# Kernel tuning notes

Measured on AMD Instinct MI355X. Metric: run time of the kernel, lower is better.

Reference implementation:

```python
import jax, jax.numpy as jnp
import numpy as np

STATIC_TH = 0.05
TRIM_RATIO = 0.2
EPS = 1e-6


def setup_inputs() -> dict:
    key = jax.random.key(0)
    k1, k2, k3 = jax.random.split(key, 3)
    B, T, H, W = 2, 32, 518, 518
    pred_disp = jax.random.uniform(k1, (B, T, H, W), jnp.float32, 0.01, 10.0)
    gt_depth = jax.random.uniform(k2, (B, T, H, W), jnp.float32, 0.1, 80.0)
    mask = jax.random.uniform(k3, (B, T, H, W)) > 0.2
    return {"pred_disp": pred_disp, "gt_depth": gt_depth, "mask": mask}


def _nanquantile_rows(vals, valid, q):
    """torch.nanquantile(dim=1, interpolation='linear') where invalid entries are NaN.
    vals: [N,Q] float, valid: [N,Q] bool. Returns [N] threshold (NaN if row empty)."""
    big = jnp.where(valid, vals, jnp.inf)          # invalid -> +inf, sorts to the end
    srt = jnp.sort(big, axis=1)                    # [N,Q]
    nv = valid.sum(axis=1)                         # valid count per row
    pos = q * jnp.maximum(nv - 1, 0).astype(vals.dtype)
    lo = jnp.floor(pos).astype(jnp.int32)
    hi = jnp.ceil(pos).astype(jnp.int32)
    frac = pos - lo.astype(vals.dtype)
    vlo = jnp.take_along_axis(srt, lo[:, None], axis=1)[:, 0]
    vhi = jnp.take_along_axis(srt, hi[:, None], axis=1)[:, 0]
    thresh = vlo * (1.0 - frac) + vhi * frac
    return jnp.where(nv > 0, thresh, jnp.nan)      # empty row -> NaN (keep-mask all False)


def reference(pred_disp, gt_depth, mask):
    B, T, H, W = pred_disp.shape
    raw = jnp.clip(pred_disp, EPS)                 # [B,T,H,W]
    gt_disp = 1.0 / jnp.clip(gt_depth, EPS)

    # per-batch least-squares scale/shift alignment on masked pixels
    raw_f = raw.reshape(B, -1)
    gt_f = gt_disp.reshape(B, -1)
    mf = mask.reshape(B, -1).astype(raw.dtype)
    count = jnp.maximum(mf.sum(axis=1, keepdims=True), 1.0)
    mean_raw = (raw_f * mf).sum(axis=1, keepdims=True) / count
    mean_gt = (gt_f * mf).sum(axis=1, keepdims=True) / count
    d_c = (raw_f - mean_raw) * mf
    g_c = (gt_f - mean_gt) * mf
    cov = (d_c * g_c).sum(axis=1, keepdims=True)
    var = jnp.maximum((d_c * d_c).sum(axis=1, keepdims=True), EPS)
    s = cov / var
    t = mean_gt - s * mean_raw
    aligned = (raw_f * s + t).reshape(B, T, H, W)

    # temporal gradient matching on static pixels
    d_diff = jnp.abs(aligned[:, 1:] - aligned[:, :-1])     # [B,T-1,H,W]
    g_diff = jnp.abs(gt_disp[:, 1:] - gt_disp[:, :-1])
    valid_pair = mask[:, 1:] & mask[:, :-1]
    depth_diff = jnp.abs(gt_depth[:, 1:] - gt_depth[:, :-1])
    static = valid_pair & (depth_diff < STATIC_TH)
    err = jnp.abs(d_diff - g_diff)

    N = B * (T - 1)
    Q = H * W
    err2 = err.reshape(N, Q)
    st2 = static.reshape(N, Q)

    # trimmed (robust) masked mean per frame pair
    thresh = _nanquantile_rows(err2, st2, 1.0 - TRIM_RATIO)   # [N]
    keep = st2 & (err2 <= thresh[:, None])
    sum_err = (err2 * keep.astype(err2.dtype)).sum(axis=1)
    cnt = jnp.maximum(keep.sum(axis=1).astype(err2.dtype), 1.0)
    loss_frame = sum_err / cnt
    return loss_frame.mean()
```

## Files before the change

kernel.cpp:

```cpp
#include <hip/hip_runtime.h>
#include <math.h>

#define HW      268324
#define HW4     67081
#define T_      32
#define B_      2
#define NPAIR   31
#define NROW    62
#define GX      263
#define NBLKB   GX
#define NF      32
#define SLOTS   5
#define CAP     2048
#define CSTR    16
#define EPSF    1e-6f
#define STH     0.05f

typedef float fx4 __attribute__((ext_vector_type(4)));
typedef int   ix4 __attribute__((ext_vector_type(4)));


__device__ __forceinline__ float fast_rcp(float x) {
    float r = __builtin_amdgcn_rcpf(x);
    float e = fmaf(-x, r, 1.0f);
    return fmaf(r, e, r);
}

__device__ __forceinline__ fx4 nt_load4(const float* p) {
    return __builtin_nontemporal_load((const fx4*)p);
}
__device__ __forceinline__ ix4 nt_load4i(const int* p) {
    return __builtin_nontemporal_load((const ix4*)p);
}
__device__ __forceinline__ unsigned int nt_loadu(const unsigned char* p) {
    return __builtin_nontemporal_load((const unsigned int*)p);
}

__device__ __forceinline__ int word_bad(unsigned int w) {
    return (w != 0u && w != 1u && w != 0xFFFFFFFFu && w != 0x3F800000u) ? 1 : 0;
}

__global__ void init_detect_kernel(const unsigned int* __restrict__ m,
                                   int* __restrict__ flag,
                                   int* __restrict__ cnt,
                                   float* __restrict__ out) {
    const int tid = threadIdx.x;
    for (int i = tid; i < NROW * CSTR; i += 256) cnt[i] = 0;
    if (tid == 0) out[0] = 0.0f;

    const unsigned int* mm = m;
    int bad = 0;
    #pragma unroll
    for (int u = 0; u < 16; ++u) {
        const unsigned int w = mm[u * 256 + tid];
        bad |= word_bad(w);
    }
    #pragma unroll
    for (int o = 32; o > 0; o >>= 1) bad |= __shfl_down(bad, o);
    __shared__ int red[4];
    const int wid = tid >> 6, lane = tid & 63;
    if (lane == 0) red[wid] = bad;
    __syncthreads();
    if (tid == 0) *flag = (red[0] | red[1] | red[2] | red[3]) ? 1 : 0;
}

__launch_bounds__(256)
__global__ void pass1_kernel(const float* __restrict__ pred,
                             const float* __restrict__ depth,
                             const void*  __restrict__ maskp,
                             const int*   __restrict__ flag,
                             double* __restrict__ partials,
                             int*    __restrict__ cnt,
                             float*  __restrict__ rbuf,
                             float*  __restrict__ gbuf)
{
    const int byteFmt = *flag;
    const int p4 = blockIdx.x * 256 + threadIdx.x;
    const bool active = (p4 < HW4);
    const int p4c = active ? p4 : (HW4 - 1);
    const int b = blockIdx.y;
    const size_t base = (size_t)b * T_ * HW + (size_t)p4c * 4;

    const float* pp = pred + base;
    const float* dd = depth + base;
    const unsigned char* m8 = (const unsigned char*)maskp + base;
    const int* m32 = (const int*)maskp + base;

    fx4 pvs[SLOTS], dvs[SLOTS];
    unsigned int mws[SLOTS];
    ix4 mis[SLOTS];

    #pragma unroll
    for (int k = 0; k < SLOTS - 1; ++k) {
        pvs[k] = nt_load4(pp + (size_t)k * HW);
        dvs[k] = nt_load4(dd + (size_t)k * HW);
        if (byteFmt) mws[k] = nt_loadu(m8 + (size_t)k * HW);
        else         mis[k] = nt_load4i(m32 + (size_t)k * HW);
    }

    int scn = 0;
    float f_r = 0.f, f_g = 0.f, f_rg = 0.f, f_rr = 0.f;
    float pcr[4], pcg[4], pcd[4];
    unsigned int pmb = 0u;

    #pragma unroll
    for (int k = 0; k < NF; ++k) {
        if (k + SLOTS - 1 < NF) {
            const int s2 = (k + SLOTS - 1) % SLOTS;
            pvs[s2] = nt_load4(pp + (size_t)(k + SLOTS - 1) * HW);
            dvs[s2] = nt_load4(dd + (size_t)(k + SLOTS - 1) * HW);
            if (byteFmt) mws[s2] = nt_loadu(m8 + (size_t)(k + SLOTS - 1) * HW);
            else         mis[s2] = nt_load4i(m32 + (size_t)(k + SLOTS - 1) * HW);
        }
        const int s = k % SLOTS;
        unsigned int mb;
        if (byteFmt) {
            const unsigned int w = mws[s];
            mb = ((w & 0x000000FFu) ? 1u : 0u) | ((w & 0x0000FF00u) ? 2u : 0u)
               | ((w & 0x00FF0000u) ? 4u : 0u) | ((w & 0xFF000000u) ? 8u : 0u);
        } else {
            const ix4 mi = mis[s];
            mb = (mi.x ? 1u : 0u) | (mi.y ? 2u : 0u) | (mi.z ? 4u : 0u) | (mi.w ? 8u : 0u);
        }
        if (!active) mb = 0u;

        const float px[4] = {pvs[s].x, pvs[s].y, pvs[s].z, pvs[s].w};
        const float dx[4] = {dvs[s].x, dvs[s].y, dvs[s].z, dvs[s].w};
        float cr[4], cg[4], cd[4];
        #pragma unroll
        for (int j = 0; j < 4; ++j) {
            cr[j] = fmaxf(px[j], EPSF);
            cd[j] = dx[j];
            cg[j] = fast_rcp(fmaxf(dx[j], EPSF));
        }

        #pragma unroll
        for (int j = 0; j < 4; ++j) {
            const bool m = (mb >> j) & 1u;
            const float rm = m ? cr[j] : 0.0f;
            const float gm = m ? cg[j] : 0.0f;
            scn += m ? 1 : 0;
            f_r += rm; f_g += gm;
            f_rg = fmaf(rm, gm, f_rg);
            f_rr = fmaf(rm, rm, f_rr);
        }

        if (k >= 1) {
            const int row = b * NPAIR + k - 1;
            #pragma unroll
            for (int j = 0; j < 4; ++j) {
                if (((mb >> j) & (pmb >> j) & 1u) && fabsf(cd[j] - pcd[j]) < STH) {
                    const int pos = atomicAdd(&cnt[row * CSTR], 1);
                    if (pos < CAP) {
                        rbuf[row * CAP + pos] = fabsf(cr[j] - pcr[j]);
                        gbuf[row * CAP + pos] = fabsf(cg[j] - pcg[j]);
                    }
                }
            }
        }

        #pragma unroll
        for (int j = 0; j < 4; ++j) { pcr[j] = cr[j]; pcg[j] = cg[j]; pcd[j] = cd[j]; }
        pmb = mb;
    }

    double v1 = (double)f_r, v2 = (double)f_g, v3 = (double)f_rg, v4 = (double)f_rr;
    int vc = scn;
    #pragma unroll
    for (int o = 32; o > 0; o >>= 1) {
        v1 += __shfl_down(v1, o); v2 += __shfl_down(v2, o);
        v3 += __shfl_down(v3, o); v4 += __shfl_down(v4, o);
        vc += __shfl_down(vc, o);
    }
    __shared__ double red[4][4];
    __shared__ int redc[4];
    const int wid = threadIdx.x >> 6, lane = threadIdx.x & 63;
    if (lane == 0) { red[wid][0]=v1; red[wid][1]=v2; red[wid][2]=v3; red[wid][3]=v4; redc[wid]=vc; }
    __syncthreads();
    if (threadIdx.x == 0) {
        double* p = partials + (size_t)(blockIdx.y * GX + blockIdx.x) * 5;
        p[0] = (double)(redc[0] + redc[1] + redc[2] + redc[3]);
        p[1] = red[0][0]+red[1][0]+red[2][0]+red[3][0];
        p[2] = red[0][1]+red[1][1]+red[2][1]+red[3][1];
        p[3] = red[0][2]+red[1][2]+red[2][2]+red[3][2];
        p[4] = red[0][3]+red[1][3]+red[2][3]+red[3][3];
    }
}

__launch_bounds__(256)
__global__ void rowquant_kernel(const double* __restrict__ partials,
                                const int* __restrict__ cnt,
                                const float* __restrict__ rbuf,
                                const float* __restrict__ gbuf,
                                float* __restrict__ out)
{
    __shared__ float arr[CAP];
    __shared__ double rs[4][5];
    __shared__ float s_sa;
    __shared__ int   s_P;
    const int row = blockIdx.x;
    const int bb  = row / NPAIR;
    const int wid = threadIdx.x >> 6, lane = threadIdx.x & 63;

    const double* p = partials + (size_t)bb * NBLKB * 5;
    double v[5] = {0, 0, 0, 0, 0};
    for (int i = threadIdx.x; i < NBLKB; i += 256) {
        #pragma unroll
        for (int j = 0; j < 5; ++j) v[j] += p[i * 5 + j];
    }
    #pragma unroll
    for (int o = 32; o > 0; o >>= 1) {
        #pragma unroll
        for (int j = 0; j < 5; ++j) v[j] += __shfl_down(v[j], o);
    }
    if (lane == 0) {
        #pragma unroll
        for (int j = 0; j < 5; ++j) rs[wid][j] = v[j];
    }
    __syncthreads();

    int n = cnt[row * CSTR]; if (n > CAP) n = CAP;
    if (threadIdx.x == 0) {
        const double c0  = rs[0][0]+rs[1][0]+rs[2][0]+rs[3][0];
        const double sr  = rs[0][1]+rs[1][1]+rs[2][1]+rs[3][1];
        const double sg  = rs[0][2]+rs[1][2]+rs[2][2]+rs[3][2];
        const double srg = rs[0][3]+rs[1][3]+rs[2][3]+rs[3][3];
        const double srr = rs[0][4]+rs[1][4]+rs[2][4]+rs[3][4];
        const double count = fmax(c0, 1.0);
        const double mr = sr / count, mg = sg / count;
        const double cov = srg - mr * sg - mg * sr + c0 * mr * mg;
        double       var = srr - 2.0 * mr * sr + c0 * mr * mr;
        var = fmax(var, 1e-6);
        s_sa = (float)fabs(cov / var);
        int P = 64; while (P < n) P <<= 1;
        s_P = P;
    }
    __syncthreads();
    const float sa = s_sa;
    const int   P  = s_P;

    for (int i = threadIdx.x; i < P; i += 256) {
        float e = INFINITY;
        if (i < n) e = fabsf(sa * rbuf[row * CAP + i] - gbuf[row * CAP + i]);
        arr[i] = e;
    }
    __syncthreads();

    for (int k = 2; k <= P; k <<= 1) {
        for (int j = k >> 1; j > 0; j >>= 1) {
            for (int i = threadIdx.x; i < P; i += 256) {
                const int ij = i ^ j;
                if (ij > i) {
                    const float a = arr[i], bv = arr[ij];
                    const bool up = ((i & k) == 0);
                    if ((a > bv) == up) { arr[i] = bv; arr[ij] = a; }
                }
            }
            __syncthreads();
        }
    }

    __shared__ float sthresh;
    if (threadIdx.x == 0) {
        if (n > 0) {
            const float pos  = 0.8f * (float)(n - 1);
            const int   lo   = (int)floorf(pos);
            const int   hi   = (int)ceilf(pos);
            const float frac = pos - (float)lo;
            sthresh = arr[lo] * (1.0f - frac) + arr[hi] * frac;
        } else {
            sthresh = -1.0f;
        }
    }
    __syncthreads();
    const float th = sthresh;

    double lsum = 0.0; int lcnt = 0;
    for (int i = threadIdx.x; i < n; i += 256) {
        const float e = arr[i];
        if (e <= th) { lsum += (double)e; lcnt++; }
    }
    #pragma unroll
    for (int o = 32; o > 0; o >>= 1) { lsum += __shfl_down(lsum, o); lcnt += __shfl_down(lcnt, o); }
    __shared__ double rr[4]; __shared__ int rc[4];
    if (lane == 0) { rr[wid] = lsum; rc[wid] = lcnt; }
    __syncthreads();
    if (threadIdx.x == 0) {
        const double tot = rr[0] + rr[1] + rr[2] + rr[3];
        const int    tc  = rc[0] + rc[1] + rc[2] + rc[3];
        const double loss_row = tot / (double)(tc > 0 ? tc : 1);
        atomicAdd(out, (float)(loss_row * (1.0 / (double)NROW)));
    }
}

extern "C" void kernel_launch(void* const* d_in, const int* in_sizes, int n_in,
                              void* d_out, int out_size, void* d_ws, size_t ws_size,
                              hipStream_t stream) {
    const float* pred  = (const float*)d_in[0];
    const float* depth = (const float*)d_in[1];
    const void*  mask  = d_in[2];
    float* out = (float*)d_out;

    char* ws = (char*)d_ws;
    int*    flag       = (int*)(ws + 0);
    int*    cnt        = (int*)(ws + 64);
    double* partials   = (double*)(ws + 8192);
    float*  rbuf       = (float*)(ws + 180224);
    float*  gbuf       = (float*)(ws + 688128);

    init_detect_kernel<<<1, 256, 0, stream>>>((const unsigned int*)mask, flag, cnt, out);
    dim3 g1(GX, B_);
    pass1_kernel<<<g1, 256, 0, stream>>>(pred, depth, mask, flag, partials, cnt, rbuf, gbuf);
    rowquant_kernel<<<NROW, 256, 0, stream>>>(partials, cnt, rbuf, gbuf, out);
}
```

Before: 223.3 us.

## Split frame loop into temporal chunks and template mask format on host

Splits each batch's 32-frame sweep into 4 chunks of 8 frames, each re-reading one overlapping frame, which launches four times as many blocks for better occupancy on the many-CU GPU. Mask format detection moves from a device kernel to a host check on input sizes, with a templated kernel and memset calls replacing the init kernel. Non-temporal loads become plain loads. The change costs roughly one extra frame read per chunk, and the partials layout must match the rowquant reduction (not shown), which may now need NBLKB=4*GX partial entries.

```diff
diff --git a/kernel.cpp b/kernel.cpp
--- a/kernel.cpp
+++ b/kernel.cpp
@@ -8,9 +8,10 @@
 #define NPAIR   31
 #define NROW    62
 #define GX      263
-#define NBLKB   GX
-#define NF      32
-#define SLOTS   5
+#define CHUNKS  4
+#define NBLKB   (CHUNKS*GX)
+#define NFC     9
+#define SLOTS   4
 #define CAP     2048
 #define CSTR    16
 #define EPSF    1e-6f
@@ -26,60 +27,28 @@
     return fmaf(r, e, r);
 }
 
-__device__ __forceinline__ fx4 nt_load4(const float* p) {
-    return __builtin_nontemporal_load((const fx4*)p);
-}
-__device__ __forceinline__ ix4 nt_load4i(const int* p) {
-    return __builtin_nontemporal_load((const ix4*)p);
-}
-__device__ __forceinline__ unsigned int nt_loadu(const unsigned char* p) {
-    return __builtin_nontemporal_load((const unsigned int*)p);
-}
-
-__device__ __forceinline__ int word_bad(unsigned int w) {
-    return (w != 0u && w != 1u && w != 0xFFFFFFFFu && w != 0x3F800000u) ? 1 : 0;
-}
-
-__global__ void init_detect_kernel(const unsigned int* __restrict__ m,
-                                   int* __restrict__ flag,
-                                   int* __restrict__ cnt,
-                                   float* __restrict__ out) {
-    const int tid = threadIdx.x;
-    for (int i = tid; i < NROW * CSTR; i += 256) cnt[i] = 0;
-    if (tid == 0) out[0] = 0.0f;
-
-    const unsigned int* mm = m;
-    int bad = 0;
-    #pragma unroll
-    for (int u = 0; u < 16; ++u) {
-        const unsigned int w = mm[u * 256 + tid];
-        bad |= word_bad(w);
-    }
-    #pragma unroll
-    for (int o = 32; o > 0; o >>= 1) bad |= __shfl_down(bad, o);
-    __shared__ int red[4];
-    const int wid = tid >> 6, lane = tid & 63;
-    if (lane == 0) red[wid] = bad;
-    __syncthreads();
-    if (tid == 0) *flag = (red[0] | red[1] | red[2] | red[3]) ? 1 : 0;
-}
-
-__launch_bounds__(256)
+__device__ __forceinline__ fx4 ld4(const float* p)          { return *(const fx4*)p; }
+__device__ __forceinline__ ix4 ld4i(const int* p)           { return *(const ix4*)p; }
+__device__ __forceinline__ unsigned int ldu(const unsigned char* p) { return *(const unsigned int*)p; }
+
+template<int BYTEFMT>
+__launch_bounds__(256, 4)
 __global__ void pass1_kernel(const float* __restrict__ pred,
                              const float* __restrict__ depth,
                              const void*  __restrict__ maskp,
-                             const int*   __restrict__ flag,
                              double* __restrict__ partials,
                              int*    __restrict__ cnt,
                              float*  __restrict__ rbuf,
                              float*  __restrict__ gbuf)
 {
-    const int byteFmt = *flag;
     const int p4 = blockIdx.x * 256 + threadIdx.x;
     const bool active = (p4 < HW4);
     const int p4c = active ? p4 : (HW4 - 1);
-    const int b = blockIdx.y;
-    const size_t base = (size_t)b * T_ * HW + (size_t)p4c * 4;
+    const int b = blockIdx.y >> 2;
+    const int c = blockIdx.y & 3;
+    const int fs = c * 8;
+    const size_t base = (size_t)b * T_ * HW + (size_t)fs * HW + (size_t)p4c * 4;
+    const size_t off8 = (size_t)((c == 3) ? 7 : 8) * HW;
 
     const float* pp = pred + base;
     const float* dd = depth + base;
@@ -92,10 +61,10 @@
 
     #pragma unroll
     for (int k = 0; k < SLOTS - 1; ++k) {
-        pvs[k] = nt_load4(pp + (size_t)k * HW);
-        dvs[k] = nt_load4(dd + (size_t)k * HW);
-        if (byteFmt) mws[k] = nt_loadu(m8 + (size_t)k * HW);
-        else         mis[k] = nt_load4i(m32 + (size_t)k * HW);
+        pvs[k] = ld4(pp + (size_t)k * HW);
+        dvs[k] = ld4(dd + (size_t)k * HW);
+        if (BYTEFMT) mws[k] = ldu(m8 + (size_t)k * HW);
+        else         mis[k] = ld4i(m32 + (size_t)k * HW);
     }
 
     int scn = 0;
@@ -104,17 +73,19 @@
     unsigned int pmb = 0u;
 
     #pragma unroll
-    for (int k = 0; k < NF; ++k) {
-        if (k + SLOTS - 1 < NF) {
-            const int s2 = (k + SLOTS - 1) % SLOTS;
-            pvs[s2] = nt_load4(pp + (size_t)(k + SLOTS - 1) * HW);
-            dvs[s2] = nt_load4(dd + (size_t)(k + SLOTS - 1) * HW);
-            if (byteFmt) mws[s2] = nt_loadu(m8 + (size_t)(k + SLOTS - 1) * HW);
-            else         mis[s2] = nt_load4i(m32 + (size_t)(k + SLOTS - 1) * HW);
+    for (int k = 0; k < NFC; ++k) {
+        const int kp = k + SLOTS - 1;
+        if (kp < NFC) {
+            const size_t off = (kp < 8) ? (size_t)kp * HW : off8;
+            const int s2 = kp % SLOTS;
+            pvs[s2] = ld4(pp + off);
+            dvs[s2] = ld4(dd + off);
+            if (BYTEFMT) mws[s2] = ldu(m8 + off);
+            else         mis[s2] = ld4i(m32 + off);
         }
         const int s = k % SLOTS;
         unsigned int mb;
-        if (byteFmt) {
+        if (BYTEFMT) {
             const unsigned int w = mws[s];
             mb = ((w & 0x000000FFu) ? 1u : 0u) | ((w & 0x0000FF00u) ? 2u : 0u)
                | ((w & 0x00FF0000u) ? 4u : 0u) | ((w & 0xFF000000u) ? 8u : 0u);
@@ -134,19 +105,21 @@
             cg[j] = fast_rcp(fmaxf(dx[j], EPSF));
         }
 
-        #pragma unroll
-        for (int j = 0; j < 4; ++j) {
-            const bool m = (mb >> j) & 1u;
-            const float rm = m ? cr[j] : 0.0f;
-            const float gm = m ? cg[j] : 0.0f;
-            scn += m ? 1 : 0;
-            f_r += rm; f_g += gm;
-            f_rg = fmaf(rm, gm, f_rg);
-            f_rr = fmaf(rm, rm, f_rr);
-        }
-
-        if (k >= 1) {
-            const int row = b * NPAIR + k - 1;
+        if (k <= 7) {
+            #pragma unroll
+            for (int j = 0; j < 4; ++j) {
+                const bool m = (mb >> j) & 1u;
+                const float rm = m ? cr[j] : 0.0f;
+                const float gm = m ? cg[j] : 0.0f;
+                scn += m ? 1 : 0;
+                f_r += rm; f_g += gm;
+                f_rg = fmaf(rm, gm, f_rg);
+                f_rr = fmaf(rm, rm, f_rr);
+            }
+        }
+
+        if (k >= 1 && (k <= 7 || c < 3)) {
+            const int row = b * NPAIR + fs + k - 1;
             #pragma unroll
             for (int j = 0; j < 4; ++j) {
                 if (((mb >> j) & (pmb >> j) & 1u) && fabsf(cd[j] - pcd[j]) < STH) {
@@ -302,14 +275,20 @@
     float* out = (float*)d_out;
 
     char* ws = (char*)d_ws;
-    int*    flag       = (int*)(ws + 0);
     int*    cnt        = (int*)(ws + 64);
     double* partials   = (double*)(ws + 8192);
     float*  rbuf       = (float*)(ws + 180224);
     float*  gbuf       = (float*)(ws + 688128);
 
-    init_detect_kernel<<<1, 256, 0, stream>>>((const unsigned int*)mask, flag, cnt, out);
-    dim3 g1(GX, B_);
-    pass1_kernel<<<g1, 256, 0, stream>>>(pred, depth, mask, flag, partials, cnt, rbuf, gbuf);
+    const int byteFmt = (in_sizes[2] != in_sizes[0]) ? 1 : 0;
+
+    hipMemsetAsync(cnt, 0, NROW * CSTR * sizeof(int), stream);
+    hipMemsetAsync(out, 0, sizeof(float), stream);
+
+    dim3 g1(GX, B_ * CHUNKS);
+    if (byteFmt)
+        pass1_kernel<1><<<g1, 256, 0, stream>>>(pred, depth, mask, partials, cnt, rbuf, gbuf);
+    else
+        pass1_kernel<0><<<g1, 256, 0, stream>>>(pred, depth, mask, partials, cnt, rbuf, gbuf);
     rowquant_kernel<<<NROW, 256, 0, stream>>>(partials, cnt, rbuf, gbuf, out);
 }
```

After: 214.4 us. 4.0% less time.
